# Optimization experiments

Measured on AMD Instinct MI355X. Metric: run time of the kernel, lower is better.

## Reference

```python
import jax, jax.numpy as jnp
import numpy as np

HEADS = 16
HEAD_DIM = 64
EMB = 1024
B, S = 4, 2048
SCALE = 1.0 / 8.0  # fixed constant in the original code
MASK_PENALTY = -50.0  # original adds -50 * upper_triangular, not -inf


def setup_inputs() -> dict:
    key = jax.random.key(0)
    ks = jax.random.split(key, 5)
    x = jax.random.normal(ks[0], (B, S, EMB), dtype=jnp.float32)
    Wq = jax.random.normal(ks[1], (EMB, HEADS * HEAD_DIM), dtype=jnp.float32) * 0.02
    Wk = jax.random.normal(ks[2], (EMB, HEADS * HEAD_DIM), dtype=jnp.float32) * 0.02
    Wv = jax.random.normal(ks[3], (EMB, HEADS * HEAD_DIM), dtype=jnp.float32) * 0.02
    Wr = jax.random.normal(ks[4], (HEADS * HEAD_DIM, EMB), dtype=jnp.float32) * 0.02
    return {"x": x, "Wq": Wq, "Wk": Wk, "Wv": Wv, "Wr": Wr}


def reference(x, Wq, Wk, Wv, Wr):
    b, s, _ = x.shape
    # project and split heads: [b, s, h, d]
    q = (x @ Wq).reshape(b, s, HEADS, HEAD_DIM)
    k = (x @ Wk).reshape(b, s, HEADS, HEAD_DIM)
    v = (x @ Wv).reshape(b, s, HEADS, HEAD_DIM)
    # scores: [b, h, s, s]
    scores = SCALE * jnp.einsum('bqhd,bkhd->bhqk', q, k)
    # causal additive mask: -50 on strictly-upper triangle (faithful to original)
    causal = jnp.triu(jnp.ones((s, s), dtype=x.dtype), k=1)
    scores = scores + MASK_PENALTY * causal
    attn = jax.nn.softmax(scores, axis=-1)
    out = jnp.einsum('bhqk,bkhd->bqhd', attn, v).reshape(b, s, HEADS * HEAD_DIM)
    return out @ Wr
```

## Files before the change

### kernel.cpp

```cpp
#include <hip/hip_runtime.h>

typedef _Float16 f16;
typedef _Float16 f16x8 __attribute__((ext_vector_type(8)));
typedef _Float16 f16x4 __attribute__((ext_vector_type(4)));
typedef float f32x4 __attribute__((ext_vector_type(4)));

#define MFMA16(A, B, C) __builtin_amdgcn_mfma_f32_16x16x32_f16((A), (B), (C), 0, 0, 0)

__device__ __forceinline__ void async16(void* lds, const void* gp) {
    __builtin_amdgcn_global_load_lds(
        (__attribute__((address_space(1))) void*)(gp),
        (__attribute__((address_space(3))) void*)(lds), 16, 0, 0);
}

__global__ __launch_bounds__(256) void k_convert(const float* __restrict__ in,
                                                 f16* __restrict__ out, int n) {
    int i = (blockIdx.x * 256 + threadIdx.x) * 4;
    if (i + 3 < n) {
        float4 v = *(const float4*)(in + i);
        f16x4 o = {(f16)v.x, (f16)v.y, (f16)v.z, (f16)v.w};
        *(f16x4*)(out + i) = o;
    }
}

__global__ __launch_bounds__(256) void k_transpose_w4(const float* __restrict__ Wq,
                                                      const float* __restrict__ Wk,
                                                      const float* __restrict__ Wv,
                                                      const float* __restrict__ Wr,
                                                      f16* __restrict__ Wqkvt,
                                                      f16* __restrict__ Wrt) {
    __shared__ float tile[32][33];
    int z = blockIdx.z;
    const float* W = (z == 0) ? Wq : (z == 1) ? Wk : (z == 2) ? Wv : Wr;
    f16* Wt = (z == 3) ? Wrt : Wqkvt + z * 1048576;
    int c0 = blockIdx.x * 32, r0 = blockIdx.y * 32;
    int tx = threadIdx.x, ty = threadIdx.y;
#pragma unroll
    for (int j = 0; j < 32; j += 8)
        tile[ty + j][tx] = W[(r0 + ty + j) * 1024 + c0 + tx];
    __syncthreads();
#pragma unroll
    for (int j = 0; j < 32; j += 8)
        Wt[(c0 + ty + j) * 1024 + r0 + tx] = (f16)tile[tx][ty + j];
}

__global__ __launch_bounds__(256) void k_transpose_v(const f16* __restrict__ QKV,
                                                     f16* __restrict__ Vt) {
    __shared__ f16 tile[32][33];
    int s0 = blockIdx.x * 32;
    int d0 = blockIdx.y * 32;
    int bh = blockIdx.z;
    int b = bh >> 4, h = bh & 15;
    int tx = threadIdx.x, ty = threadIdx.y;
#pragma unroll
    for (int j = 0; j < 32; j += 8)
        tile[ty + j][tx] = QKV[(b * 2048 + s0 + ty + j) * 3072 + 2048 + h * 64 + d0 + tx];
    __syncthreads();
#pragma unroll
    for (int j = 0; j < 32; j += 8)
        Vt[(bh * 64 + d0 + ty + j) * 2048 + s0 + tx] = tile[tx][ty + j];
}

template <bool OUT_F16>
__global__ __launch_bounds__(256) void k_gemm_bt(const f16* __restrict__ A,
                                                 const f16* __restrict__ Bt,
                                                 void* __restrict__ Cv,
                                                 int M, int N, int K) {
    __shared__ f16 As[128][32];
    __shared__ f16 Bs[128][32];
    int t = threadIdx.x;
    int lane = t & 63, w = t >> 6;
    int wm = (w >> 1) * 64, wn = (w & 1) * 64;
    int m0 = blockIdx.y * 128, n0 = blockIdx.x * 128;
    int ln = lane & 15, g = lane >> 4;

    int lin0 = w * 128 + lane, lin1 = lin0 + 64;
    int r0 = lin0 >> 2, c0 = (lin0 & 3) ^ ((r0 >> 1) & 3);
    int r1 = lin1 >> 2, c1 = (lin1 & 3) ^ ((r1 >> 1) & 3);
    const f16* gA0 = A + (size_t)(m0 + r0) * K + c0 * 8;
    const f16* gA1 = A + (size_t)(m0 + r1) * K + c1 * 8;
    const f16* gB0 = Bt + (size_t)(n0 + r0) * K + c0 * 8;
    const f16* gB1 = Bt + (size_t)(n0 + r1) * K + c1 * 8;
    f16* lA0 = &As[0][0] + w * 1024;
    f16* lB0 = &Bs[0][0] + w * 1024;

    f32x4 acc[4][4] = {};
    int sw = (ln >> 1) & 3;

    for (int k0 = 0; k0 < K; k0 += 32) {
        __syncthreads();
        async16(lA0, gA0 + k0);
        async16(lA0 + 512, gA1 + k0);
        async16(lB0, gB0 + k0);
        async16(lB0 + 512, gB1 + k0);
        __syncthreads();
        f16x8 af[4], bf[4];
#pragma unroll
        for (int i = 0; i < 4; i++) {
            af[i] = *(const f16x8*)&As[wm + i * 16 + ln][(g ^ sw) * 8];
            bf[i] = *(const f16x8*)&Bs[wn + i * 16 + ln][(g ^ sw) * 8];
        }
#pragma unroll
        for (int mt = 0; mt < 4; mt++)
#pragma unroll
            for (int nt = 0; nt < 4; nt++)
                acc[mt][nt] = MFMA16(af[mt], bf[nt], acc[mt][nt]);
    }

    int rg = g * 4;
#pragma unroll
    for (int mt = 0; mt < 4; mt++)
#pragma unroll
        for (int nt = 0; nt < 4; nt++)
#pragma unroll
            for (int r = 0; r < 4; r++) {
                int row = m0 + wm + mt * 16 + rg + r;
                int col = n0 + wn + nt * 16 + ln;
                float v = acc[mt][nt][r];
                if (OUT_F16)
                    ((f16*)Cv)[(size_t)row * N + col] = (f16)v;
                else
                    ((float*)Cv)[(size_t)row * N + col] = v;
            }
}

__global__ __launch_bounds__(256, 2) void k_attn(const f16* __restrict__ QKV,
                                                 const f16* __restrict__ Vt,
                                                 f16* __restrict__ Opart,
                                                 float* __restrict__ Rsum) {
    __shared__ f16 Ks[2][64][72];
    __shared__ f16 Vs[2][64][72];
    int bh = blockIdx.x, pi = blockIdx.y;
    int b = bh >> 4, h = bh & 15;
    int t = threadIdx.x, lane = t & 63, wq = t >> 6;
    int ln = lane & 15, g = lane >> 4, g8 = g * 8, rg = g * 4;

    int kr0 = t >> 3, kc0 = (t & 7) * 8;
    int kr1 = kr0 + 32;
    int kg0 = ((kr0 & 16) >> 2) | ((kr0 & 12) << 1) | (kr0 & 3);
    int kg1 = kg0 + 32;
    const f16* Kbase = QKV + (size_t)b * 2048 * 3072 + 1024 + h * 64;
    const f16* Vbase = Vt + (size_t)bh * 64 * 2048;

    const float C_SCL = 0.18033688f;
    const float C_MSK = -72.134752f;
    f16x8 ones;
#pragma unroll
    for (int j = 0; j < 8; j++) ones[j] = (f16)1.f;

    int nk0 = 16 - pi;

    int4 rk0, rk1, rv0, rv1;
#define LOADT(j)                                                          \
    do {                                                                  \
        int j_ = (j);                                                     \
        int kt_ = (j_ < nk0) ? j_ : j_ - nk0 + pi + 1;                    \
        size_t kO = (size_t)kt_ * 64;                                     \
        rk0 = *(const int4*)(Kbase + (kO + kg0) * 3072 + kc0);            \
        rk1 = *(const int4*)(Kbase + (kO + kg1) * 3072 + kc0);            \
        rv0 = *(const int4*)(Vbase + (size_t)kr0 * 2048 + kO + kc0);      \
        rv1 = *(const int4*)(Vbase + (size_t)kr1 * 2048 + kO + kc0);      \
    } while (0)
#define STORET(bi)                                                        \
    do {                                                                  \
        *(int4*)&Ks[bi][kr0][kc0] = rk0;                                  \
        *(int4*)&Ks[bi][kr1][kc0] = rk1;                                  \
        *(int4*)&Vs[bi][kr0][kc0] = rv0;                                  \
        *(int4*)&Vs[bi][kr1][kc0] = rv1;                                  \
    } while (0)

    LOADT(0);
    STORET(0);
    LOADT(1);
    __syncthreads();

    int i = 0;
    for (int phase = 0; phase < 2; phase++) {
        int qt  = phase ? pi : 15 - pi;
        int ktB = phase ? pi + 1 : 0;
        int ktE = phase ? 2 * pi + 2 : 16 - pi;
        int q0 = qt * 128;

        f16x8 bq[2][2];
#pragma unroll
        for (int nt = 0; nt < 2; nt++)
#pragma unroll
            for (int kd = 0; kd < 2; kd++)
                bq[nt][kd] = *(const f16x8*)(QKV +
                    (size_t)(b * 2048 + q0 + wq * 32 + nt * 16 + ln) * 3072 +
                    h * 64 + kd * 32 + g8);

        f32x4 oacc[2][4] = {};
        f32x4 osum[2] = {};

        for (int kt = ktB; kt < ktE; kt++, i++) {
            int cur = i & 1;
            int k0 = kt * 64;
            bool active = (k0 <= q0 + wq * 32 + 31);

            f16x8 ak[2][4];
            if (active) {
#pragma unroll
                for (int kd = 0; kd < 2; kd++)
#pragma unroll
                    for (int mt = 0; mt < 4; mt++)
                        ak[kd][mt] = *(const f16x8*)&Ks[cur][mt * 16 + ln][kd * 32 + g8];
            }
            if (i + 1 < 17) STORET(cur ^ 1);
            if (i + 2 < 17) LOADT(i + 2);

            if (active) {
                f32x4 sacc[4][2] = {};
#pragma unroll
                for (int kd = 0; kd < 2; kd++)
#pragma unroll
                    for (int mt = 0; mt < 4; mt++)
#pragma unroll
                        for (int nt = 0; nt < 2; nt++)
                            sacc[mt][nt] = MFMA16(ak[kd][mt], bq[nt][kd], sacc[mt][nt]);

                bool needs_mask = (k0 + 63 > q0 + wq * 32);
                f16x8 ap[2][2];
#pragma unroll
                for (int nt = 0; nt < 2; nt++) {
                    int q = q0 + wq * 32 + nt * 16 + ln;
#pragma unroll
                    for (int mt = 0; mt < 4; mt++) {
                        int kb = mt >> 1, hi4 = (mt & 1) * 4;
#pragma unroll
                        for (int r = 0; r < 4; r++) {
                            float e;
                            if (needs_mask) {
                                int kk = k0 + kb * 32 + hi4 + 8 * g + r;
                                e = __builtin_amdgcn_exp2f(
                                    fmaf(sacc[mt][nt][r], C_SCL, (kk > q) ? C_MSK : 0.f));
                            } else {
                                e = __builtin_amdgcn_exp2f(sacc[mt][nt][r] * C_SCL);
                            }
                            ap[nt][kb][hi4 + r] = (f16)e;
                        }
                    }
                }

#pragma unroll
                for (int kk = 0; kk < 2; kk++) {
                    f16x8 bv[4];
#pragma unroll
                    for (int dt = 0; dt < 4; dt++)
                        bv[dt] = *(const f16x8*)&Vs[cur][dt * 16 + ln][kk * 32 + g8];
#pragma unroll
                    for (int nt = 0; nt < 2; nt++) {
#pragma unroll
                        for (int dt = 0; dt < 4; dt++)
                            oacc[nt][dt] = MFMA16(ap[nt][kk], bv[dt], oacc[nt][dt]);
                        osum[nt] = MFMA16(ap[nt][kk], ones, osum[nt]);
                    }
                }
            }
            __syncthreads();
        }

        int u = (bh * 16 + qt) * 2 + phase;
#pragma unroll
        for (int nt = 0; nt < 2; nt++)
#pragma unroll
            for (int r = 0; r < 4; r++) {
                float rs = osum[nt][r];
                float inv = __builtin_amdgcn_rcpf(fmaxf(rs, 1e-30f));
                int q = wq * 32 + nt * 16 + rg + r;
                if (ln == 0) Rsum[u * 128 + q] = rs;
#pragma unroll
                for (int dt = 0; dt < 4; dt++)
                    Opart[(size_t)u * 8192 + q * 64 + dt * 16 + ln] =
                        (f16)(oacc[nt][dt][r] * inv);
            }
    }
#undef LOADT
#undef STORET
}

__global__ __launch_bounds__(256) void k_merge(const f16* __restrict__ Op,
                                               const float* __restrict__ Rs,
                                               f16* __restrict__ Ob) {
    int idx = blockIdx.x * 256 + threadIdx.x;
    int d8 = idx & 7;
    int q  = (idx >> 3) & 127;
    int qt = (idx >> 10) & 15;
    int bh = idx >> 14;
    int b = bh >> 4, hd = bh & 15;
    int u0 = (bh * 16 + qt) * 2;
    float rs0 = Rs[u0 * 128 + q], rs1 = Rs[(u0 + 1) * 128 + q];
    float inv = __builtin_amdgcn_rcpf(rs0 + rs1);
    f16x8 o0 = *(const f16x8*)(Op + (size_t)u0 * 8192 + q * 64 + d8 * 8);
    f16x8 o1 = *(const f16x8*)(Op + (size_t)(u0 + 1) * 8192 + q * 64 + d8 * 8);
    f16x8 o;
#pragma unroll
    for (int j = 0; j < 8; j++)
        o[j] = (f16)((rs0 * (float)o0[j] + rs1 * (float)o1[j]) * inv);
    *(f16x8*)(Ob + (size_t)(b * 2048 + qt * 128 + q) * 1024 + hd * 64 + d8 * 8) = o;
}

extern "C" void kernel_launch(void* const* d_in, const int* in_sizes, int n_in,
                              void* d_out, int out_size, void* d_ws, size_t ws_size,
                              hipStream_t stream) {
    const float* x = (const float*)d_in[0];
    const float* Wq = (const float*)d_in[1];
    const float* Wk = (const float*)d_in[2];
    const float* Wv = (const float*)d_in[3];
    const float* Wr = (const float*)d_in[4];
    float* out = (float*)d_out;

    f16* ws = (f16*)d_ws;
    f16* xb    = ws;
    f16* Wqkvt = xb + 8388608;
    f16* Wrt   = Wqkvt + 3145728;
    f16* QKVb  = Wrt + 1048576;
    f16* Vtb   = QKVb + 25165824;
    f16* Obuf  = Vtb + 8388608;
    f16* Opart = Obuf + 8388608;
    float* Rsum = (float*)(Opart + 16777216);

    k_convert<<<8192, 256, 0, stream>>>(x, xb, 8388608);
    dim3 tb(32, 8);
    k_transpose_w4<<<dim3(32, 32, 4), tb, 0, stream>>>(Wq, Wk, Wv, Wr, Wqkvt, Wrt);
    k_gemm_bt<true><<<dim3(24, 64), 256, 0, stream>>>(xb, Wqkvt, QKVb, 8192, 3072, 1024);
    k_transpose_v<<<dim3(64, 2, 64), tb, 0, stream>>>(QKVb, Vtb);
    k_attn<<<dim3(64, 16), 256, 0, stream>>>(QKVb, Vtb, Opart, Rsum);
    k_merge<<<4096, 256, 0, stream>>>(Opart, Rsum, Obuf);
    k_gemm_bt<false><<<dim3(8, 64), 256, 0, stream>>>(Obuf, Wrt, out, 8192, 1024, 1024);
}
```

Baseline: 291.8 us.

## Load attention K/V tiles straight into LDS asynchronously with XOR swizzle

Replaces the register-staged global→register→LDS K/V tile copies with direct global_load_lds async copies into a double buffer. The padded LDS rows are replaced by an XOR-swizzled layout so the fragment reads avoid bank conflicts. This frees registers and removes the explicit store step, with the aim of better overlap and occupancy. The prefetch depth drops from two tiles ahead to one, which could expose more load latency.

```diff
diff --git a/kernel.cpp b/kernel.cpp
--- a/kernel.cpp
+++ b/kernel.cpp
@@ -128,19 +128,24 @@
                                                  const f16* __restrict__ Vt,
                                                  f16* __restrict__ Opart,
                                                  float* __restrict__ Rsum) {
-    __shared__ f16 Ks[2][64][72];
-    __shared__ f16 Vs[2][64][72];
+    __shared__ f16 Ks[2][64][64];
+    __shared__ f16 Vs[2][64][64];
     int bh = blockIdx.x, pi = blockIdx.y;
     int b = bh >> 4, h = bh & 15;
     int t = threadIdx.x, lane = t & 63, wq = t >> 6;
     int ln = lane & 15, g = lane >> 4, g8 = g * 8, rg = g * 4;
-
-    int kr0 = t >> 3, kc0 = (t & 7) * 8;
-    int kr1 = kr0 + 32;
-    int kg0 = ((kr0 & 16) >> 2) | ((kr0 & 12) << 1) | (kr0 & 3);
-    int kg1 = kg0 + 32;
-    const f16* Kbase = QKV + (size_t)b * 2048 * 3072 + 1024 + h * 64;
-    const f16* Vbase = Vt + (size_t)bh * 64 * 2048;
+    int sx = ln & 7;
+
+    int r0 = wq * 8 + (lane >> 3);
+    int cp = lane & 7;
+    int cl = (cp ^ (r0 & 7)) * 8;
+    int gk0 = ((r0 & 16) >> 2) | ((r0 & 12) << 1) | (r0 & 3);
+    const f16* Kb = QKV + (size_t)b * 2048 * 3072 + 1024 + h * 64;
+    const f16* Vb = Vt + (size_t)bh * 64 * 2048;
+    const f16* gK0 = Kb + (size_t)gk0 * 3072 + cl;
+    const f16* gK1 = Kb + (size_t)(gk0 + 32) * 3072 + cl;
+    const f16* gV0 = Vb + (size_t)r0 * 2048 + cl;
+    const f16* gV1 = Vb + (size_t)(r0 + 32) * 2048 + cl;
 
     const float C_SCL = 0.18033688f;
     const float C_MSK = -72.134752f;
@@ -150,28 +155,18 @@
 
     int nk0 = 16 - pi;
 
-    int4 rk0, rk1, rv0, rv1;
-#define LOADT(j)                                                          \
+#define ISSUE(bi, j)                                                      \
     do {                                                                  \
-        int j_ = (j);                                                     \
-        int kt_ = (j_ < nk0) ? j_ : j_ - nk0 + pi + 1;                    \
+        int jj = (j);                                                     \
+        int kt_ = (jj < nk0) ? jj : jj - nk0 + pi + 1;                    \
         size_t kO = (size_t)kt_ * 64;                                     \
-        rk0 = *(const int4*)(Kbase + (kO + kg0) * 3072 + kc0);            \
-        rk1 = *(const int4*)(Kbase + (kO + kg1) * 3072 + kc0);            \
-        rv0 = *(const int4*)(Vbase + (size_t)kr0 * 2048 + kO + kc0);      \
-        rv1 = *(const int4*)(Vbase + (size_t)kr1 * 2048 + kO + kc0);      \
+        async16(&Ks[bi][wq * 8][0],      gK0 + kO * 3072);                \
+        async16(&Ks[bi][32 + wq * 8][0], gK1 + kO * 3072);                \
+        async16(&Vs[bi][wq * 8][0],      gV0 + kO);                       \
+        async16(&Vs[bi][32 + wq * 8][0], gV1 + kO);                       \
     } while (0)
-#define STORET(bi)                                                        \
-    do {                                                                  \
-        *(int4*)&Ks[bi][kr0][kc0] = rk0;                                  \
-        *(int4*)&Ks[bi][kr1][kc0] = rk1;                                  \
-        *(int4*)&Vs[bi][kr0][kc0] = rv0;                                  \
-        *(int4*)&Vs[bi][kr1][kc0] = rv1;                                  \
-    } while (0)
-
-    LOADT(0);
-    STORET(0);
-    LOADT(1);
+
+    ISSUE(0, 0);
     __syncthreads();
 
     int i = 0;
@@ -198,18 +193,16 @@
             int k0 = kt * 64;
             bool active = (k0 <= q0 + wq * 32 + 31);
 
-            f16x8 ak[2][4];
+            if (i + 1 < 17) ISSUE(cur ^ 1, i + 1);
+
             if (active) {
+                f16x8 ak[2][4];
 #pragma unroll
                 for (int kd = 0; kd < 2; kd++)
 #pragma unroll
                     for (int mt = 0; mt < 4; mt++)
-                        ak[kd][mt] = *(const f16x8*)&Ks[cur][mt * 16 + ln][kd * 32 + g8];
-            }
-            if (i + 1 < 17) STORET(cur ^ 1);
-            if (i + 2 < 17) LOADT(i + 2);
-
-            if (active) {
+                        ak[kd][mt] = *(const f16x8*)
+                            &Ks[cur][mt * 16 + ln][((kd * 4 + g) ^ sx) * 8];
                 f32x4 sacc[4][2] = {};
 #pragma unroll
                 for (int kd = 0; kd < 2; kd++)
@@ -247,7 +240,8 @@
                     f16x8 bv[4];
 #pragma unroll
                     for (int dt = 0; dt < 4; dt++)
-                        bv[dt] = *(const f16x8*)&Vs[cur][dt * 16 + ln][kk * 32 + g8];
+                        bv[dt] = *(const f16x8*)
+                            &Vs[cur][dt * 16 + ln][((kk * 4 + g) ^ sx) * 8];
 #pragma unroll
                     for (int nt = 0; nt < 2; nt++) {
 #pragma unroll
@@ -275,8 +269,7 @@
                         (f16)(oacc[nt][dt][r] * inv);
             }
     }
-#undef LOADT
-#undef STORET
+#undef ISSUE
 }
 
 __global__ __launch_bounds__(256) void k_merge(const f16* __restrict__ Op,
```

Result: faster. 285.5 us (-2.2%).
